# Optimization experiments

Measured on AMD Instinct MI355X. Metric: run time of the kernel, lower is better.

The kernel has to match this reference:

```python
import jax, jax.numpy as jnp
import numpy as np

B, S, D, E = 16, 2048, 1024, 1024
NEG = -1e13  # not_mask_sign from the original module


def setup_inputs() -> dict:
    key = jax.random.key(0)
    k1, k2, k3, k4, k5, k6 = jax.random.split(key, 6)
    return {
        "Q": jax.random.normal(k1, (B, S, D), dtype=jnp.float32),
        "K": jax.random.normal(k2, (B, S, D), dtype=jnp.float32),
        "V": jax.random.normal(k3, (B, S, D), dtype=jnp.float32),
        "pad_idxs": jax.random.randint(k4, (B,), 0, S, dtype=jnp.int64),
        "W": jax.random.normal(k5, (D, E), dtype=jnp.float32) * (1.0 / np.sqrt(D)),
        "b": jax.random.normal(k6, (E,), dtype=jnp.float32) * 0.01,
    }


def reference(Q, K, V, pad_idxs, W, b):
    d = Q.shape[2]
    # [B, S, S] attention scores
    scores = jnp.einsum("bqd,bkd->bqk", Q, K) / jnp.sqrt(jnp.asarray(d, Q.dtype))
    # Faithful to original: mask entries where row>=pad AND col>=pad
    idx = jnp.arange(scores.shape[1])
    p = pad_idxs[:, None, None]
    mask = (idx[None, :, None] >= p) & (idx[None, None, :] >= p)  # [B,S,S]
    scores = jnp.where(mask, jnp.asarray(NEG, scores.dtype), scores)
    attn = jax.nn.softmax(scores, axis=2)
    out = jnp.einsum("bqk,bkd->bqd", attn, V)
    return out @ W + b
```

## Files before the change

### kernel.cpp

```cpp
#include <hip/hip_runtime.h>

typedef unsigned short u16;
typedef unsigned int u32;
typedef long long ll;
typedef __attribute__((ext_vector_type(8))) short bf16x8;
typedef __attribute__((ext_vector_type(8))) unsigned short u16x8;
typedef __attribute__((ext_vector_type(4))) float f32x4;

__device__ __forceinline__ u16 f2bf(float f) {
  u32 x = __float_as_uint(f);
  x += 0x7fffu + ((x >> 16) & 1u);
  return (u16)(x >> 16);
}
__device__ __forceinline__ float bf2f(u16 u) {
  return __uint_as_float(((u32)u) << 16);
}

__device__ __forceinline__ int read_pad(const int* pw, int z) {
  int odd = pw[1] | pw[3] | pw[5] | pw[7] | pw[9] | pw[11] | pw[13] | pw[15];
  return (odd == 0) ? pw[2 * z] : pw[z];
}

template<int ROWS>
__device__ __forceinline__ void stage_unit(const u16* gsrc, int gld, u16* dst,
                                           int wid, int lane) {
  const int rsub = lane >> 2;
  const int gk = ((lane & 3) ^ ((lane >> 3) & 3)) * 8;
#pragma unroll
  for (int q = 0; q < ROWS / 128; ++q) {
    const int r0 = (q * 8 + wid) * 16;
    __builtin_amdgcn_global_load_lds(
        (const __attribute__((address_space(1))) void*)(gsrc + (ll)(r0 + rsub) * gld + gk),
        (__attribute__((address_space(3))) void*)(dst + r0 * 32),
        16, 0, 0);
  }
}

template<int EPI>
__global__ __launch_bounds__(512, 4) void gemm8(
    const u16* __restrict__ A, const u16* __restrict__ B, void* __restrict__ C,
    int Kdim, int lda, int ldb, int ldc, ll sA, ll sB, ll sC,
    const int* __restrict__ pad, const float* __restrict__ bias,
    float* __restrict__ lsum, int NX, int NXY, int nwg) {
  __shared__ __align__(16) u16 ldsA[2][256 * 32];
  __shared__ __align__(16) u16 ldsB[2][128 * 32];

  const int orig = blockIdx.x;
  const int q8 = nwg >> 3, r8 = nwg & 7;
  const int xcd = orig & 7, inner = orig >> 3;
  const int wg = (xcd < r8 ? xcd * (q8 + 1) : r8 * (q8 + 1) + (xcd - r8) * q8) + inner;
  const int z = wg / NXY;
  const int rem = wg - z * NXY;
  const int by = rem / NX;
  const int bx = rem - by * NX;

  const int tid = threadIdx.x;
  const int wid = tid >> 6, lane = tid & 63;
  const int lr = lane & 15, lg = lane >> 4;
  const int wr = wid >> 2;
  const int wn32 = (wid & 3) * 32;
  const int bm = by * 256, bn = bx * 128;
  const u16* Ab = A + (ll)z * sA + (ll)bm * lda;
  const u16* Bb = B + (ll)z * sB + (ll)bn * ldb;

  const int aoff = lr * 32 + ((lg ^ ((lr >> 1) & 3)) * 8);

  f32x4 acc[8][2];
#pragma unroll
  for (int i = 0; i < 8; ++i)
#pragma unroll
    for (int j = 0; j < 2; ++j) acc[i][j] = (f32x4)0.0f;

  const int NT = Kdim >> 5;

  stage_unit<256>(Ab, lda, &ldsA[0][0], wid, lane);
  stage_unit<128>(Bb, ldb, &ldsB[0][0], wid, lane);
  asm volatile("s_waitcnt vmcnt(0)" ::: "memory");
  __builtin_amdgcn_s_barrier();

  for (int t = 0; t < NT; ++t) {
    const int c = t & 1;
    if (t + 1 < NT) {
      stage_unit<256>(Ab + (ll)(t + 1) * 32, lda, &ldsA[c ^ 1][0], wid, lane);
      stage_unit<128>(Bb + (ll)(t + 1) * 32, ldb, &ldsB[c ^ 1][0], wid, lane);
    }
    bf16x8 bv[2], av[4];
#pragma unroll
    for (int i = 0; i < 2; ++i)
      bv[i] = *(const bf16x8*)(&ldsB[c][0] + (wn32 + i * 16) * 32 + aoff);
#pragma unroll
    for (int i = 0; i < 4; ++i)
      av[i] = *(const bf16x8*)(&ldsA[c][0] + (wr * 128 + i * 16) * 32 + aoff);
    __builtin_amdgcn_s_setprio(1);
#pragma unroll
    for (int i = 0; i < 4; ++i)
#pragma unroll
      for (int j = 0; j < 2; ++j)
        acc[i][j] = __builtin_amdgcn_mfma_f32_16x16x32_bf16(av[i], bv[j],
                                                            acc[i][j], 0, 0, 0);
    __builtin_amdgcn_s_setprio(0);
#pragma unroll
    for (int i = 0; i < 4; ++i)
      av[i] = *(const bf16x8*)(&ldsA[c][0] + (wr * 128 + (4 + i) * 16) * 32 + aoff);
    __builtin_amdgcn_s_setprio(1);
#pragma unroll
    for (int i = 0; i < 4; ++i)
#pragma unroll
      for (int j = 0; j < 2; ++j)
        acc[4 + i][j] = __builtin_amdgcn_mfma_f32_16x16x32_bf16(
            av[i], bv[j], acc[4 + i][j], 0, 0, 0);
    __builtin_amdgcn_s_setprio(0);
    asm volatile("s_waitcnt vmcnt(0)" ::: "memory");
    __builtin_amdgcn_s_barrier();
  }

  int p = 0;
  if constexpr (EPI == 0) p = read_pad(pad, z);
#pragma unroll
  for (int mf = 0; mf < 8; ++mf) {
#pragma unroll
    for (int rg = 0; rg < 4; ++rg) {
      const int row = bm + wr * 128 + mf * 16 + 4 * lg + rg;
      if constexpr (EPI == 0) {
        float part = 0.0f;
#pragma unroll
        for (int nf = 0; nf < 2; ++nf) {
          const int col = bn + wn32 + nf * 16 + lr;
          float e;
          if (row >= p && col >= p) e = (p == 0) ? 1.0f : 0.0f;
          else e = __expf(acc[mf][nf][rg] * 0.03125f);
          part += e;
          ((u16*)C)[(ll)z * sC + (ll)row * ldc + col] = f2bf(e);
        }
        part += __shfl_xor(part, 1);
        part += __shfl_xor(part, 2);
        part += __shfl_xor(part, 4);
        part += __shfl_xor(part, 8);
        if (lr == 0) atomicAdd(&lsum[z * 2048 + row], part);
      } else if constexpr (EPI == 3) {
        const float linv = 1.0f / lsum[z * 2048 + row];
#pragma unroll
        for (int nf = 0; nf < 2; ++nf) {
          const int col = bn + wn32 + nf * 16 + lr;
          ((u16*)C)[(ll)z * sC + (ll)row * ldc + col] =
              f2bf(acc[mf][nf][rg] * linv);
        }
      } else {
#pragma unroll
        for (int nf = 0; nf < 2; ++nf) {
          const int col = bn + wn32 + nf * 16 + lr;
          if constexpr (EPI == 1) {
            ((u16*)C)[(ll)z * sC + (ll)row * ldc + col] = f2bf(acc[mf][nf][rg]);
          } else {
            ((float*)C)[(ll)z * sC + (ll)row * ldc + col] =
                acc[mf][nf][rg] + bias[col];
          }
        }
      }
    }
  }
}

__global__ __launch_bounds__(256) void zerof(float* __restrict__ p) {
  p[blockIdx.x * 256 + threadIdx.x] = 0.0f;
}

__global__ __launch_bounds__(256) void cvt_bf16(const float* __restrict__ src,
                                                u16* __restrict__ dst) {
  const ll i = ((ll)blockIdx.x * 256 + threadIdx.x) * 8;
  const float4 a = *(const float4*)(src + i);
  const float4 b = *(const float4*)(src + i + 4);
  u16x8 v;
  v[0] = f2bf(a.x); v[1] = f2bf(a.y); v[2] = f2bf(a.z); v[3] = f2bf(a.w);
  v[4] = f2bf(b.x); v[5] = f2bf(b.y); v[6] = f2bf(b.z); v[7] = f2bf(b.w);
  *(u16x8*)(dst + i) = v;
}

__global__ __launch_bounds__(256) void transpose_cvt(
    const float* __restrict__ src, u16* __restrict__ dst, int R, int C,
    ll sS, ll sD) {
  __shared__ u16 t[64][65];
  const int tid = threadIdx.x;
  const int r0 = blockIdx.y * 64, c0 = blockIdx.x * 64;
  const float* s = src + (ll)blockIdx.z * sS;
  u16* d = dst + (ll)blockIdx.z * sD;
#pragma unroll
  for (int it = 0; it < 16; ++it) {
    const int idx = it * 256 + tid;
    const int r = idx >> 6, c = idx & 63;
    t[r][c] = f2bf(s[(ll)(r0 + r) * C + c0 + c]);
  }
  __syncthreads();
#pragma unroll
  for (int it = 0; it < 16; ++it) {
    const int idx = it * 256 + tid;
    const int rr = idx >> 6, cc = idx & 63;
    d[(ll)(c0 + rr) * R + r0 + cc] = t[cc][rr];
  }
}

__global__ __launch_bounds__(256) void softmax_rows(u16* __restrict__ P,
                                                    const int* __restrict__ pad) {
  const int wid = threadIdx.x >> 6, lane = threadIdx.x & 63;
  const ll row = (ll)blockIdx.x * 4 + wid;
  const int z = (int)(row >> 11);
  const int r = (int)(row & 2047);
  const int p = read_pad(pad, z);
  const bool rmask = (r >= p);
  u16* ptr = P + row * 2048;
  float s[32];
#pragma unroll
  for (int i = 0; i < 4; ++i) {
    const u16x8 v = *(const u16x8*)(ptr + i * 512 + lane * 8);
#pragma unroll
    for (int j = 0; j < 8; ++j) {
      const int col = i * 512 + lane * 8 + j;
      float x = bf2f(v[j]) * 0.03125f;
      if (rmask && col >= p) x = -1e13f;
      s[i * 8 + j] = x;
    }
  }
  float m = s[0];
#pragma unroll
  for (int i = 1; i < 32; ++i) m = fmaxf(m, s[i]);
#pragma unroll
  for (int o = 1; o < 64; o <<= 1) m = fmaxf(m, __shfl_xor(m, o));
  float sum = 0.0f;
#pragma unroll
  for (int i = 0; i < 32; ++i) {
    s[i] = __expf(s[i] - m);
    sum += s[i];
  }
#pragma unroll
  for (int o = 1; o < 64; o <<= 1) sum += __shfl_xor(sum, o);
  const float inv = 1.0f / sum;
#pragma unroll
  for (int i = 0; i < 4; ++i) {
    u16x8 v;
#pragma unroll
    for (int j = 0; j < 8; ++j) v[j] = f2bf(s[i * 8 + j] * inv);
    *(u16x8*)(ptr + i * 512 + lane * 8) = v;
  }
}

__device__ __forceinline__ void stage_f32(const float* src, ll base, int ld,
                                          u16* lds, int tid) {
#pragma unroll
  for (int p = 0; p < 4; ++p) {
    int chunk = p * 256 + tid;
    int r = chunk >> 3, slot = chunk & 7;
    const float* s = src + base + (ll)r * ld + slot * 8;
    const float4 a = *(const float4*)s;
    const float4 b = *(const float4*)(s + 4);
    u16x8 v;
    v[0] = f2bf(a.x); v[1] = f2bf(a.y); v[2] = f2bf(a.z); v[3] = f2bf(a.w);
    v[4] = f2bf(b.x); v[5] = f2bf(b.y); v[6] = f2bf(b.z); v[7] = f2bf(b.w);
    *(u16x8*)(lds + r * 64 + (slot ^ (r & 7)) * 8) = v;
  }
}

__global__ __launch_bounds__(256) void gemm_f32in(
    const float* __restrict__ A, const float* __restrict__ B,
    u16* __restrict__ C, int Kdim, int lda, int ldb, int ldc,
    ll sA, ll sB, ll sC) {
  __shared__ __align__(16) u16 As[128 * 64];
  __shared__ __align__(16) u16 Bs[128 * 64];
  const int tid = threadIdx.x;
  const int z = blockIdx.z;
  const int bm = blockIdx.y * 128, bn = blockIdx.x * 128;
  const ll abase = (ll)z * sA + (ll)bm * lda;
  const ll bbase = (ll)z * sB + (ll)bn * ldb;
  const int wid = tid >> 6, lane = tid & 63;
  const int wm = (wid >> 1) * 64, wn = (wid & 1) * 64;
  const int lr = lane & 15, lg = lane >> 4;

  f32x4 acc[4][4];
#pragma unroll
  for (int i = 0; i < 4; ++i)
#pragma unroll
    for (int j = 0; j < 4; ++j) acc[i][j] = (f32x4)0.0f;

  for (int k0 = 0; k0 < Kdim; k0 += 64) {
    __syncthreads();
    stage_f32(A, abase + k0, lda, As, tid);
    stage_f32(B, bbase + k0, ldb, Bs, tid);
    __syncthreads();
#pragma unroll
    for (int kk = 0; kk < 2; ++kk) {
      bf16x8 av[4], bv[4];
#pragma unroll
      for (int i = 0; i < 4; ++i) {
        const int ra = wm + i * 16 + lr;
        av[i] = *(const bf16x8*)(As + ra * 64 + (((kk * 4 + lg) ^ (ra & 7)) * 8));
        const int rb = wn + i * 16 + lr;
        bv[i] = *(const bf16x8*)(Bs + rb * 64 + (((kk * 4 + lg) ^ (rb & 7)) * 8));
      }
#pragma unroll
      for (int i = 0; i < 4; ++i)
#pragma unroll
        for (int j = 0; j < 4; ++j)
          acc[i][j] = __builtin_amdgcn_mfma_f32_16x16x32_bf16(av[i], bv[j],
                                                              acc[i][j], 0, 0, 0);
    }
  }
#pragma unroll
  for (int i = 0; i < 4; ++i) {
    const int rowb = bm + wm + i * 16 + 4 * lg;
#pragma unroll
    for (int j = 0; j < 4; ++j) {
      const int col = bn + wn + j * 16 + lr;
#pragma unroll
      for (int rg = 0; rg < 4; ++rg)
        C[(ll)z * sC + (ll)(rowb + rg) * ldc + col] = f2bf(acc[i][j][rg]);
    }
  }
}

extern "C" void kernel_launch(void* const* d_in, const int* in_sizes, int n_in,
                              void* d_out, int out_size, void* d_ws,
                              size_t ws_size, hipStream_t stream) {
  const float* Q = (const float*)d_in[0];
  const float* Km = (const float*)d_in[1];
  const float* V = (const float*)d_in[2];
  const int* pad = (const int*)d_in[3];
  const float* W = (const float*)d_in[4];
  const float* bias = (const float*)d_in[5];
  float* out = (float*)d_out;

  const int B = 16, S = 2048, D = 1024, E = 1024;
  const ll SS = (ll)S * S, SD = (ll)S * D;

  u16* P = (u16*)d_out;
  char* ws = (char*)d_ws;

  const size_t MB64 = (size_t)B * S * D * 2;
  const size_t szWt = (size_t)D * E * 2;
  const size_t szL = (size_t)B * S * 4;

  if (ws_size >= 3 * MB64 + szWt + szL) {
    u16* Qb = (u16*)ws;
    u16* Kb = (u16*)(ws + MB64);
    u16* Vt = (u16*)(ws + 2 * MB64);
    u16* Wt = (u16*)(ws + 3 * MB64);
    float* lsum = (float*)(ws + 3 * MB64 + szWt);
    u16* X = Qb;

    const int nv = (int)(((ll)B * S * D) / (8 * 256));
    zerof<<<dim3(B * S / 256), 256, 0, stream>>>(lsum);
    cvt_bf16<<<nv, 256, 0, stream>>>(Q, Qb);
    cvt_bf16<<<nv, 256, 0, stream>>>(Km, Kb);
    transpose_cvt<<<dim3(D / 64, S / 64, B), 256, 0, stream>>>(V, Vt, S, D, SD, SD);
    transpose_cvt<<<dim3(E / 64, D / 64, 1), 256, 0, stream>>>(W, Wt, D, E, 0, 0);

    gemm8<0><<<dim3(2048), 512, 0, stream>>>(
        Qb, Kb, P, D, D, D, S, SD, SD, SS, pad, nullptr, lsum, 16, 128, 2048);
    gemm8<3><<<dim3(1024), 512, 0, stream>>>(
        P, Vt, X, S, S, S, D, SS, SD, SD, nullptr, nullptr, lsum, 8, 64, 1024);
    gemm8<2><<<dim3(1024), 512, 0, stream>>>(
        X, Wt, out, D, D, D, E, 0, 0, 0, nullptr, bias, nullptr, 8, 1024, 1024);
  } else if (ws_size >= 2 * MB64 + szWt) {
    u16* Vt = (u16*)ws;
    u16* Wt = (u16*)(ws + MB64);
    u16* X = (u16*)(ws + MB64 + szWt);

    transpose_cvt<<<dim3(D / 64, S / 64, B), 256, 0, stream>>>(V, Vt, S, D, SD, SD);
    transpose_cvt<<<dim3(E / 64, D / 64, 1), 256, 0, stream>>>(W, Wt, D, E, 0, 0);
    gemm_f32in<<<dim3(S / 128, S / 128, B), 256, 0, stream>>>(
        Q, Km, P, D, D, D, S, SD, SD, SS);
    softmax_rows<<<dim3(B * S / 4), 256, 0, stream>>>(P, pad);
    gemm8<1><<<dim3(1024), 512, 0, stream>>>(
        P, Vt, X, S, S, S, D, SS, SD, SD, nullptr, nullptr, nullptr, 8, 64, 1024);
    gemm8<2><<<dim3(1024), 512, 0, stream>>>(
        X, Wt, out, D, D, D, E, 0, 0, 0, nullptr, bias, nullptr, 8, 1024, 1024);
  } else {
    u16* Wt = (u16*)ws;
    u16* Vtb = (u16*)(ws + szWt);
    u16* X = (u16*)(ws + szWt + (size_t)D * S * 2);

    transpose_cvt<<<dim3(E / 64, D / 64, 1), 256, 0, stream>>>(W, Wt, D, E, 0, 0);
    gemm_f32in<<<dim3(S / 128, S / 128, B), 256, 0, stream>>>(
        Q, Km, P, D, D, D, S, SD, SD, SS);
    softmax_rows<<<dim3(B * S / 4), 256, 0, stream>>>(P, pad);
    for (int b = 0; b < B; ++b) {
      transpose_cvt<<<dim3(D / 64, S / 64, 1), 256, 0, stream>>>(
          V + (ll)b * SD, Vtb, S, D, 0, 0);
      gemm8<1><<<dim3(64), 512, 0, stream>>>(
          P + (ll)b * SS, Vtb, X + (ll)b * SD, S, S, S, D, 0, 0, 0, nullptr,
          nullptr, nullptr, 8, 64, 64);
    }
    gemm8<2><<<dim3(1024), 512, 0, stream>>>(
        X, Wt, out, D, D, D, E, 0, 0, 0, nullptr, bias, nullptr, 8, 1024, 1024);
  }
}
```

Baseline: 640.9 us.

## Replace 256x128 double-buffered GEMM with single-buffered 128x128 BK64 tiles

```diff
diff --git a/kernel.cpp b/kernel.cpp
--- a/kernel.cpp
+++ b/kernel.cpp
@@ -21,29 +21,14 @@
   return (odd == 0) ? pw[2 * z] : pw[z];
 }
 
-template<int ROWS>
-__device__ __forceinline__ void stage_unit(const u16* gsrc, int gld, u16* dst,
-                                           int wid, int lane) {
-  const int rsub = lane >> 2;
-  const int gk = ((lane & 3) ^ ((lane >> 3) & 3)) * 8;
-#pragma unroll
-  for (int q = 0; q < ROWS / 128; ++q) {
-    const int r0 = (q * 8 + wid) * 16;
-    __builtin_amdgcn_global_load_lds(
-        (const __attribute__((address_space(1))) void*)(gsrc + (ll)(r0 + rsub) * gld + gk),
-        (__attribute__((address_space(3))) void*)(dst + r0 * 32),
-        16, 0, 0);
-  }
-}
-
 template<int EPI>
-__global__ __launch_bounds__(512, 4) void gemm8(
+__global__ __launch_bounds__(256, 4) void g128(
     const u16* __restrict__ A, const u16* __restrict__ B, void* __restrict__ C,
     int Kdim, int lda, int ldb, int ldc, ll sA, ll sB, ll sC,
     const int* __restrict__ pad, const float* __restrict__ bias,
     float* __restrict__ lsum, int NX, int NXY, int nwg) {
-  __shared__ __align__(16) u16 ldsA[2][256 * 32];
-  __shared__ __align__(16) u16 ldsB[2][128 * 32];
+  __shared__ __align__(16) u16 As[128 * 64];
+  __shared__ __align__(16) u16 Bs[128 * 64];
 
   const int orig = blockIdx.x;
   const int q8 = nwg >> 3, r8 = nwg & 7;
@@ -57,75 +42,65 @@
   const int tid = threadIdx.x;
   const int wid = tid >> 6, lane = tid & 63;
   const int lr = lane & 15, lg = lane >> 4;
-  const int wr = wid >> 2;
-  const int wn32 = (wid & 3) * 32;
-  const int bm = by * 256, bn = bx * 128;
+  const int wm = (wid >> 1) * 64, wn = (wid & 1) * 64;
+  const int bm = by * 128, bn = bx * 128;
   const u16* Ab = A + (ll)z * sA + (ll)bm * lda;
   const u16* Bb = B + (ll)z * sB + (ll)bn * ldb;
 
-  const int aoff = lr * 32 + ((lg ^ ((lr >> 1) & 3)) * 8);
-
-  f32x4 acc[8][2];
-#pragma unroll
-  for (int i = 0; i < 8; ++i)
-#pragma unroll
-    for (int j = 0; j < 2; ++j) acc[i][j] = (f32x4)0.0f;
-
-  const int NT = Kdim >> 5;
-
-  stage_unit<256>(Ab, lda, &ldsA[0][0], wid, lane);
-  stage_unit<128>(Bb, ldb, &ldsB[0][0], wid, lane);
-  asm volatile("s_waitcnt vmcnt(0)" ::: "memory");
-  __builtin_amdgcn_s_barrier();
-
+  f32x4 acc[4][4];
+#pragma unroll
+  for (int i = 0; i < 4; ++i)
+#pragma unroll
+    for (int j = 0; j < 4; ++j) acc[i][j] = (f32x4)0.0f;
+
+  const int NT = Kdim >> 6;
   for (int t = 0; t < NT; ++t) {
-    const int c = t & 1;
-    if (t + 1 < NT) {
-      stage_unit<256>(Ab + (ll)(t + 1) * 32, lda, &ldsA[c ^ 1][0], wid, lane);
-      stage_unit<128>(Bb + (ll)(t + 1) * 32, ldb, &ldsB[c ^ 1][0], wid, lane);
-    }
-    bf16x8 bv[2], av[4];
-#pragma unroll
-    for (int i = 0; i < 2; ++i)
-      bv[i] = *(const bf16x8*)(&ldsB[c][0] + (wn32 + i * 16) * 32 + aoff);
-#pragma unroll
-    for (int i = 0; i < 4; ++i)
-      av[i] = *(const bf16x8*)(&ldsA[c][0] + (wr * 128 + i * 16) * 32 + aoff);
-    __builtin_amdgcn_s_setprio(1);
-#pragma unroll
-    for (int i = 0; i < 4; ++i)
-#pragma unroll
-      for (int j = 0; j < 2; ++j)
-        acc[i][j] = __builtin_amdgcn_mfma_f32_16x16x32_bf16(av[i], bv[j],
-                                                            acc[i][j], 0, 0, 0);
-    __builtin_amdgcn_s_setprio(0);
-#pragma unroll
-    for (int i = 0; i < 4; ++i)
-      av[i] = *(const bf16x8*)(&ldsA[c][0] + (wr * 128 + (4 + i) * 16) * 32 + aoff);
-    __builtin_amdgcn_s_setprio(1);
-#pragma unroll
-    for (int i = 0; i < 4; ++i)
-#pragma unroll
-      for (int j = 0; j < 2; ++j)
-        acc[4 + i][j] = __builtin_amdgcn_mfma_f32_16x16x32_bf16(
-            av[i], bv[j], acc[4 + i][j], 0, 0, 0);
-    __builtin_amdgcn_s_setprio(0);
-    asm volatile("s_waitcnt vmcnt(0)" ::: "memory");
-    __builtin_amdgcn_s_barrier();
+    __syncthreads();
+#pragma unroll
+    for (int i = 0; i < 4; ++i) {
+      const int chunk = i * 256 + tid;
+      const int r = chunk >> 3;
+      const int slot = chunk & 7;
+      const int gk = t * 64 + ((slot ^ (r & 7)) * 8);
+      __builtin_amdgcn_global_load_lds(
+          (const __attribute__((address_space(1))) void*)(Ab + (ll)r * lda + gk),
+          (__attribute__((address_space(3))) void*)(As + chunk * 8), 16, 0, 0);
+      __builtin_amdgcn_global_load_lds(
+          (const __attribute__((address_space(1))) void*)(Bb + (ll)r * ldb + gk),
+          (__attribute__((address_space(3))) void*)(Bs + chunk * 8), 16, 0, 0);
+    }
+    __syncthreads();
+#pragma unroll
+    for (int kk = 0; kk < 2; ++kk) {
+      bf16x8 av[4], bv[4];
+#pragma unroll
+      for (int i = 0; i < 4; ++i) {
+        const int ra = wm + i * 16 + lr;
+        av[i] = *(const bf16x8*)(As + ra * 64 + (((kk * 4 + lg) ^ (ra & 7)) * 8));
+        const int rb = wn + i * 16 + lr;
+        bv[i] = *(const bf16x8*)(Bs + rb * 64 + (((kk * 4 + lg) ^ (rb & 7)) * 8));
+      }
+#pragma unroll
+      for (int i = 0; i < 4; ++i)
+#pragma unroll
+        for (int j = 0; j < 4; ++j)
+          acc[i][j] = __builtin_amdgcn_mfma_f32_16x16x32_bf16(av[i], bv[j],
+                                                              acc[i][j], 0, 0, 0);
+    }
   }
 
   int p = 0;
   if constexpr (EPI == 0) p = read_pad(pad, z);
 #pragma unroll
-  for (int mf = 0; mf < 8; ++mf) {
+  for (int mf = 0; mf < 4; ++mf) {
 #pragma unroll
     for (int rg = 0; rg < 4; ++rg) {
-      const int row = bm + wr * 128 + mf * 16 + 4 * lg + rg;
+      const int row = bm + wm + mf * 16 + 4 * lg + rg;
       if constexpr (EPI == 0) {
         float part = 0.0f;
 #pragma unroll
-        for (int nf = 0; nf < 2; ++nf) {
-          const int col = bn + wn32 + nf * 16 + lr;
+        for (int nf = 0; nf < 4; ++nf) {
+          const int col = bn + wn + nf * 16 + lr;
           float e;
           if (row >= p && col >= p) e = (p == 0) ? 1.0f : 0.0f;
           else e = __expf(acc[mf][nf][rg] * 0.03125f);
@@ -140,15 +115,15 @@
       } else if constexpr (EPI == 3) {
         const float linv = 1.0f / lsum[z * 2048 + row];
 #pragma unroll
-        for (int nf = 0; nf < 2; ++nf) {
-          const int col = bn + wn32 + nf * 16 + lr;
+        for (int nf = 0; nf < 4; ++nf) {
+          const int col = bn + wn + nf * 16 + lr;
           ((u16*)C)[(ll)z * sC + (ll)row * ldc + col] =
               f2bf(acc[mf][nf][rg] * linv);
         }
       } else {
 #pragma unroll
-        for (int nf = 0; nf < 2; ++nf) {
-          const int col = bn + wn32 + nf * 16 + lr;
+        for (int nf = 0; nf < 4; ++nf) {
+          const int col = bn + wn + nf * 16 + lr;
           if constexpr (EPI == 1) {
             ((u16*)C)[(ll)z * sC + (ll)row * ldc + col] = f2bf(acc[mf][nf][rg]);
           } else {
@@ -352,12 +327,12 @@
     transpose_cvt<<<dim3(D / 64, S / 64, B), 256, 0, stream>>>(V, Vt, S, D, SD, SD);
     transpose_cvt<<<dim3(E / 64, D / 64, 1), 256, 0, stream>>>(W, Wt, D, E, 0, 0);
 
-    gemm8<0><<<dim3(2048), 512, 0, stream>>>(
-        Qb, Kb, P, D, D, D, S, SD, SD, SS, pad, nullptr, lsum, 16, 128, 2048);
-    gemm8<3><<<dim3(1024), 512, 0, stream>>>(
-        P, Vt, X, S, S, S, D, SS, SD, SD, nullptr, nullptr, lsum, 8, 64, 1024);
-    gemm8<2><<<dim3(1024), 512, 0, stream>>>(
-        X, Wt, out, D, D, D, E, 0, 0, 0, nullptr, bias, nullptr, 8, 1024, 1024);
+    g128<0><<<dim3(4096), 256, 0, stream>>>(
+        Qb, Kb, P, D, D, D, S, SD, SD, SS, pad, nullptr, lsum, 16, 256, 4096);
+    g128<3><<<dim3(2048), 256, 0, stream>>>(
+        P, Vt, X, S, S, S, D, SS, SD, SD, nullptr, nullptr, lsum, 8, 128, 2048);
+    g128<2><<<dim3(2048), 256, 0, stream>>>(
+        X, Wt, out, D, D, D, E, 0, 0, 0, nullptr, bias, nullptr, 8, 2048, 2048);
   } else if (ws_size >= 2 * MB64 + szWt) {
     u16* Vt = (u16*)ws;
     u16* Wt = (u16*)(ws + MB64);
@@ -368,10 +343,10 @@
     gemm_f32in<<<dim3(S / 128, S / 128, B), 256, 0, stream>>>(
         Q, Km, P, D, D, D, S, SD, SD, SS);
     softmax_rows<<<dim3(B * S / 4), 256, 0, stream>>>(P, pad);
-    gemm8<1><<<dim3(1024), 512, 0, stream>>>(
-        P, Vt, X, S, S, S, D, SS, SD, SD, nullptr, nullptr, nullptr, 8, 64, 1024);
-    gemm8<2><<<dim3(1024), 512, 0, stream>>>(
-        X, Wt, out, D, D, D, E, 0, 0, 0, nullptr, bias, nullptr, 8, 1024, 1024);
+    g128<1><<<dim3(2048), 256, 0, stream>>>(
+        P, Vt, X, S, S, S, D, SS, SD, SD, nullptr, nullptr, nullptr, 8, 128, 2048);
+    g128<2><<<dim3(2048), 256, 0, stream>>>(
+        X, Wt, out, D, D, D, E, 0, 0, 0, nullptr, bias, nullptr, 8, 2048, 2048);
   } else {
     u16* Wt = (u16*)ws;
     u16* Vtb = (u16*)(ws + szWt);
@@ -384,11 +359,11 @@
     for (int b = 0; b < B; ++b) {
       transpose_cvt<<<dim3(D / 64, S / 64, 1), 256, 0, stream>>>(
           V + (ll)b * SD, Vtb, S, D, 0, 0);
-      gemm8<1><<<dim3(64), 512, 0, stream>>>(
+      g128<1><<<dim3(128), 256, 0, stream>>>(
           P + (ll)b * SS, Vtb, X + (ll)b * SD, S, S, S, D, 0, 0, 0, nullptr,
-          nullptr, nullptr, 8, 64, 64);
-    }
-    gemm8<2><<<dim3(1024), 512, 0, stream>>>(
-        X, Wt, out, D, D, D, E, 0, 0, 0, nullptr, bias, nullptr, 8, 1024, 1024);
-  }
-}
+          nullptr, nullptr, 8, 128, 128);
+    }
+    g128<2><<<dim3(2048), 256, 0, stream>>>(
+        X, Wt, out, D, D, D, E, 0, 0, 0, nullptr, bias, nullptr, 8, 2048, 2048);
+  }
+}
```

Result: faster. 532.7 us (-16.9%).
